# Optimization experiments

Measured on AMD Instinct MI355X. Metric: run time of the kernel, lower is better.

## Reference

```python
import jax, jax.numpy as jnp
import numpy as np

C = 128
NUM_GROUPS = 32  # min(32, 128 // 4)
EPS = 1e-6


def group_norm(x, gamma, beta):
    N, Cc, H, W = x.shape
    xg = x.reshape(N, NUM_GROUPS, -1)
    mean = xg.mean(axis=-1, keepdims=True)
    var = ((xg - mean) ** 2).mean(axis=-1, keepdims=True)
    xn = ((xg - mean) * jax.lax.rsqrt(var + EPS)).reshape(N, Cc, H, W)
    return xn * gamma[None, :, None, None] + beta[None, :, None, None]


def conv1x1(x, w, b):
    # w: [C_out, C_in], b: [C_out]; 1x1 conv == channel matmul
    return jnp.einsum('nchw,oc->nohw', x, w) + b[None, :, None, None]


def setup_inputs() -> dict:
    key = jax.random.key(0)
    ks = jax.random.split(key, 11)
    s = 1.0 / np.sqrt(C)
    return {
        'x': jax.random.normal(ks[0], (4, C, 64, 64), dtype=jnp.float32),
        'gamma': jnp.ones((C,), jnp.float32),
        'beta': jnp.zeros((C,), jnp.float32),
        'wq': jax.random.normal(ks[1], (C, C), jnp.float32) * s,
        'bq': jnp.zeros((C,), jnp.float32),
        'wk': jax.random.normal(ks[2], (C, C), jnp.float32) * s,
        'bk': jnp.zeros((C,), jnp.float32),
        'wv': jax.random.normal(ks[3], (C, C), jnp.float32) * s,
        'bv': jnp.zeros((C,), jnp.float32),
        'wo': jax.random.normal(ks[4], (C, C), jnp.float32) * s,
        'bo': jnp.zeros((C,), jnp.float32),
    }


def reference(x, gamma, beta, wq, bq, wk, bk, wv, bv, wo, bo):
    N, Cc, H, W = x.shape
    L = H * W
    xn = group_norm(x, gamma, beta)
    q = conv1x1(xn, wq, bq).reshape(N, Cc, L)  # [N,C,L]
    k = conv1x1(xn, wk, bk).reshape(N, Cc, L)
    v = conv1x1(xn, wv, bv).reshape(N, Cc, L)
    scale = 1.0 / jnp.sqrt(jnp.asarray(Cc, x.dtype))
    scores = jnp.einsum('ncl,ncm->nlm', q, k) * scale  # [N,L,L]
    weights = jax.nn.softmax(scores, axis=-1)
    attn = jnp.einsum('nlm,ncm->ncl', weights, v).reshape(N, Cc, H, W)
    return x + conv1x1(attn, wo, bo)
```

## Files before the change

kernel.cpp:

```cpp
#include <hip/hip_runtime.h>
#include <hip/hip_bf16.h>


#define N_B 4
#define C_D 128
#define L_D 4096
#define SPLIT 4
#define KVB 128
#define FSTEPS ((L_D/SPLIT)/KVB)
#define QSCALE (0.08838834764831845f * 1.4426950408889634f)
#define FIXM 16.0f

using f32x4  = __attribute__((ext_vector_type(4))) float;
using f32x16 = __attribute__((ext_vector_type(16))) float;
using bf16x8 = __attribute__((ext_vector_type(8))) short;

static __device__ __forceinline__ unsigned short f2bf(float f){
  return (unsigned short)((__builtin_bit_cast(unsigned int, f) + 0x8000u) >> 16);
}
static __device__ __forceinline__ float bf2f(unsigned short u){
  unsigned int x = ((unsigned int)u) << 16;
  return __builtin_bit_cast(float, x);
}
static __device__ __forceinline__ unsigned int pk2(float a, float b){
  unsigned int ua = __builtin_bit_cast(unsigned int, a) + 0x8000u;
  unsigned int ub = __builtin_bit_cast(unsigned int, b) + 0x8000u;
  return __builtin_amdgcn_perm(ub, ua, 0x07060302u);
}
static __device__ __forceinline__ float exp2a(float x){
  float r; asm("v_exp_f32 %0, %1" : "=v"(r) : "v"(x)); return r;
}
static __device__ __forceinline__ void gll16(const void* g, void* l){
  __builtin_amdgcn_global_load_lds(
      (const __attribute__((address_space(1))) unsigned int*)g,
      (__attribute__((address_space(3))) unsigned int*)l, 16, 0, 0);
}

__global__ __launch_bounds__(256) void gnw_k(
    const float* __restrict__ x, float* __restrict__ stats,
    const float* __restrict__ wq, const float* __restrict__ wk,
    const float* __restrict__ wv, const float* __restrict__ wo,
    unsigned short* __restrict__ wbf)
{
  int b = blockIdx.x, t = threadIdx.x;
  if (b >= 128){
    int b2 = b - 128;
    int mat = b2 >> 4;
    const float* src = (mat == 0) ? wq : (mat == 1) ? wk : (mat == 2) ? wv : wo;
    int off = (b2 & 15) * 1024 + t * 4;
    float4 v = *(const float4*)(src + off);
    *(uint2*)(wbf + mat*16384 + off) = make_uint2(pk2(v.x, v.y), pk2(v.z, v.w));
    return;
  }
  const float4* p = (const float4*)(x + (size_t)b * (4 * L_D));
  float s = 0.f, ss = 0.f;
#pragma unroll
  for (int i = 0; i < 16; ++i){
    float4 v = p[t + i*256];
    s  += v.x + v.y + v.z + v.w;
    ss += v.x*v.x + v.y*v.y + v.z*v.z + v.w*v.w;
  }
#pragma unroll
  for (int off = 32; off > 0; off >>= 1){
    s  += __shfl_down(s, off);
    ss += __shfl_down(ss, off);
  }
  __shared__ float rs4[4], rss4[4];
  if ((t & 63) == 0){ rs4[t>>6] = s; rss4[t>>6] = ss; }
  __syncthreads();
  if (t == 0){
    s  = rs4[0]+rs4[1]+rs4[2]+rs4[3];
    ss = rss4[0]+rss4[1]+rss4[2]+rss4[3];
    float mean = s * (1.f/16384.f);
    float var  = ss * (1.f/16384.f) - mean*mean;
    if (var < 0.f) var = 0.f;
    stats[2*b]   = mean;
    stats[2*b+1] = rsqrtf(var + 1e-6f);
  }
}

__global__ __launch_bounds__(256) void qkv_k(
    const float* __restrict__ x, const float* __restrict__ stats,
    const float* __restrict__ gamma, const float* __restrict__ beta,
    const unsigned short* __restrict__ wbf,
    const float* __restrict__ bq, const float* __restrict__ bk,
    const float* __restrict__ bv,
    unsigned short* __restrict__ q_ws, unsigned short* __restrict__ k_ws,
    unsigned short* __restrict__ v_ws)
{
  __shared__ unsigned short xnT[64][136];
  __shared__ unsigned short qbuf[64][136];

  int t = threadIdx.x, b = blockIdx.x;
  int wi = b >> 8;
  int bt = b & 255;
  int n = bt >> 6, l0 = (bt & 63) * 64;

  {
    int l = t & 63, cq = t >> 6;
#pragma unroll
    for (int it = 0; it < 8; ++it){
      int c0 = cq*4 + it*16;
      int g  = c0 >> 2;
      float mean = stats[(n*32+g)*2];
      float rstd = stats[(n*32+g)*2+1];
      float vv[4];
#pragma unroll
      for (int jj = 0; jj < 4; ++jj){
        int c = c0 + jj;
        float sc = rstd * gamma[c];
        float bs = beta[c] - mean * sc;
        vv[jj] = x[(size_t)(n*C_D + c)*L_D + l0 + l]*sc + bs;
      }
      *(unsigned int*)&xnT[l][c0]   = pk2(vv[0], vv[1]);
      *(unsigned int*)&xnT[l][c0+2] = pk2(vv[2], vv[3]);
    }
  }
  __syncthreads();

  int w = t >> 6, lane = t & 63, u = lane >> 4, l15 = lane & 15;
  int wc = w >> 1, wl = w & 1;
  const unsigned short* W = wbf + wi*16384;
  const float* Bv = (wi == 0) ? bq : (wi == 1) ? bk : bv;

  f32x4 zz = {0.f,0.f,0.f,0.f};
  f32x4 acc[4][2];
#pragma unroll
  for (int ct = 0; ct < 4; ++ct)
#pragma unroll
    for (int lt = 0; lt < 2; ++lt) acc[ct][lt] = zz;

#pragma unroll
  for (int kst = 0; kst < 4; ++kst){
    bf16x8 bfrag[2];
#pragma unroll
    for (int lt = 0; lt < 2; ++lt)
      bfrag[lt] = *(const bf16x8*)&xnT[32*wl + 16*lt + l15][kst*32 + 8*u];
#pragma unroll
    for (int ct = 0; ct < 4; ++ct){
      bf16x8 af = *(const bf16x8*)(W + (size_t)(64*wc + 16*ct + l15)*C_D + kst*32 + 8*u);
#pragma unroll
      for (int lt = 0; lt < 2; ++lt)
        acc[ct][lt] = __builtin_amdgcn_mfma_f32_16x16x32_bf16(af, bfrag[lt], acc[ct][lt], 0, 0, 0);
    }
  }

  if (wi < 2){
    float qs = (wi == 0) ? QSCALE : 1.0f;
#pragma unroll
    for (int ct = 0; ct < 4; ++ct){
      float bias[4];
#pragma unroll
      for (int r = 0; r < 4; ++r) bias[r] = Bv[64*wc + 16*ct + 4*u + r];
#pragma unroll
      for (int lt = 0; lt < 2; ++lt){
        float v0 = (acc[ct][lt][0] + bias[0]) * qs;
        float v1 = (acc[ct][lt][1] + bias[1]) * qs;
        float v2 = (acc[ct][lt][2] + bias[2]) * qs;
        float v3 = (acc[ct][lt][3] + bias[3]) * qs;
        int row = 32*wl + 16*lt + l15;
        int col = 64*wc + 16*ct + 4*u;
        *(unsigned int*)&qbuf[row][col]   = pk2(v0, v1);
        *(unsigned int*)&qbuf[row][col+2] = pk2(v2, v3);
      }
    }
    __syncthreads();
    {
      int l = t >> 2, ch = t & 3;
      unsigned short* dst = ((wi == 0) ? q_ws : k_ws) + (size_t)(n*L_D + l0 + l)*C_D + ch*32;
#pragma unroll
      for (int i = 0; i < 4; ++i)
        *(uint4*)(dst + i*8) = *(const uint4*)&qbuf[l][ch*32 + i*8];
    }
  } else {
    int p16 = (l15 & 3) | ((l15 & 4) << 1) | ((l15 & 8) >> 1);
#pragma unroll
    for (int ct = 0; ct < 4; ++ct){
      float bias[4];
#pragma unroll
      for (int r = 0; r < 4; ++r) bias[r] = Bv[64*wc + 16*ct + 4*u + r];
#pragma unroll
      for (int lt = 0; lt < 2; ++lt)
#pragma unroll
        for (int r = 0; r < 4; ++r){
          int co = 64*wc + 16*ct + 4*u + r;
          v_ws[(size_t)(n*C_D + co)*L_D + l0 + 32*wl + 16*lt + p16] =
              f2bf(acc[ct][lt][r] + bias[r]);
        }
    }
  }
}

__global__ __launch_bounds__(512, 2) void flash_split_k(
    const unsigned short* __restrict__ q_ws, const unsigned short* __restrict__ k_ws,
    const unsigned short* __restrict__ v_ws,
    unsigned short* __restrict__ po_ws, float* __restrict__ md_ws)
{
  __shared__ __align__(16) char shmem[131072];

  int t = threadIdx.x;
  int phys = blockIdx.x;
  int xcd = phys & 7, j = phys >> 3;
  int pair = xcd*8 + (j & 7);
  int s = j >> 3;
  int n = pair >> 4, lt256 = pair & 15;
  int l0 = lt256 * 256;
  int m_base = s * (L_D / SPLIT);
  int w = t >> 6, lane = t & 63, hi = lane >> 5, l31 = lane & 31;
  int lr = lane >> 4, ls = lane & 15;

  bf16x8 qf[8];
  {
    const unsigned short* qrow = q_ws + ((size_t)(n*L_D + l0 + 32*w + l31))*C_D;
#pragma unroll
    for (int kst = 0; kst < 8; ++kst)
      qf[kst] = *(const bf16x8*)(qrow + 16*kst + 8*hi);
  }

  f32x16 zz16;
#pragma unroll
  for (int i = 0; i < 16; ++i) zz16[i] = 0.f;
  f32x16 accO[4];
#pragma unroll
  for (int ct = 0; ct < 4; ++ct) accO[ct] = zz16;
  float rsum = 0.f;

  const unsigned short* kg[4];
  const unsigned short* vg[4];
  int ldof[4];
#pragma unroll
  for (int i = 0; i < 4; ++i){
    int row = 16*w + 4*i + lr;
    int ub = (ls << 4) ^ ((row & 15) << 4);
    kg[i] = k_ws + ((size_t)(n*L_D + m_base + row))*C_D + (ub >> 1);
    vg[i] = v_ws + ((size_t)(n*C_D + row))*L_D + m_base + (ub >> 1);
    ldof[i] = (16*w + 4*i)*256;
  }

  {
#pragma unroll
    for (int i = 0; i < 4; ++i){
      gll16(kg[i], shmem + ldof[i]);
      gll16(vg[i], shmem + 65536 + ldof[i]);
    }
  }
  __syncthreads();

#pragma unroll 2
  for (int step = 0; step < FSTEPS; ++step){
    int cur = step & 1, nxt = cur ^ 1;
    char* kB = shmem + (cur << 15);
    char* vB = shmem + 65536 + (cur << 15);

    if (step + 1 < FSTEPS){
      char* kN = shmem + (nxt << 15);
      char* vN = shmem + 65536 + (nxt << 15);
#pragma unroll
      for (int i = 0; i < 4; ++i){
        gll16(kg[i] + (size_t)(step+1)*KVB*C_D, kN + ldof[i]);
        gll16(vg[i] + (step+1)*KVB,             vN + ldof[i]);
      }
    }

    f32x16 accS[4];
#pragma unroll
    for (int mt = 0; mt < 4; ++mt) accS[mt] = zz16;
    __builtin_amdgcn_s_setprio(1);
#pragma unroll
    for (int mt = 0; mt < 4; ++mt){
      int row = 32*mt + l31;
      bf16x8 afr[8];
#pragma unroll
      for (int kst = 0; kst < 8; ++kst)
        afr[kst] = *(const bf16x8*)(kB + row*256 + ((32*kst + 16*hi) ^ ((row & 15) << 4)));
#pragma unroll
      for (int kst = 0; kst < 8; ++kst)
        accS[mt] = __builtin_amdgcn_mfma_f32_32x32x16_bf16(afr[kst], qf[kst], accS[mt], 0, 0, 0);
    }
    __builtin_amdgcn_s_setprio(0);

    union { unsigned int u[8]; bf16x8 h[2]; } Wm[4];
#pragma unroll
    for (int mt = 0; mt < 4; ++mt){
      float p[16];
#pragma unroll
      for (int r = 0; r < 16; ++r){ p[r] = exp2a(accS[mt][r] - FIXM); rsum += p[r]; }
#pragma unroll
      for (int wd = 0; wd < 8; ++wd) Wm[mt].u[wd] = pk2(p[2*wd], p[2*wd+1]);
    }

    __builtin_amdgcn_s_setprio(1);
#pragma unroll
    for (int sl = 0; sl < 8; ++sl){
      bf16x8 pf = Wm[sl >> 1].h[sl & 1];
      bf16x8 vfr[4];
#pragma unroll
      for (int ct = 0; ct < 4; ++ct){
        int vr = 32*ct + l31;
        vfr[ct] = *(const bf16x8*)(vB + vr*256 + ((32*sl + 16*hi) ^ ((vr & 15) << 4)));
      }
#pragma unroll
      for (int ct = 0; ct < 4; ++ct)
        accO[ct] = __builtin_amdgcn_mfma_f32_32x32x16_bf16(vfr[ct], pf, accO[ct], 0, 0, 0);
    }
    __builtin_amdgcn_s_setprio(0);
    __syncthreads();
  }

  rsum += __shfl_xor(rsum, 32);

  char* tB = shmem;
  {
    int lloc = 32*w + l31;
    int tsw = (lloc & 15) << 4;
    char* tr = tB + (size_t)lloc*256;
#pragma unroll
    for (int ct = 0; ct < 4; ++ct)
#pragma unroll
      for (int q = 0; q < 4; ++q){
        int cb2 = 64*ct + 16*q + 8*hi;
        *(unsigned int*)(tr + ((cb2    ) ^ tsw)) = pk2(accO[ct][4*q+0], accO[ct][4*q+1]);
        *(unsigned int*)(tr + ((cb2 + 4) ^ tsw)) = pk2(accO[ct][4*q+2], accO[ct][4*q+3]);
      }
  }
  __syncthreads();
  {
    int row2 = t >> 1, hf2 = t & 1;
    int tile = row2 >> 7, lrow = row2 & 127;
    size_t pb = ((size_t)((n*32 + 2*lt256 + tile)*SPLIT + s)) * (size_t)(128*128);
    unsigned short* dst = po_ws + pb + (size_t)lrow*128 + hf2*64;
    const char* srcr = tB + row2*256;
    int sw2 = (row2 & 15) << 4;
#pragma unroll
    for (int i = 0; i < 8; ++i)
      *(uint4*)(dst + 8*i) = *(const uint4*)(srcr + ((hf2*128 + 16*i) ^ sw2));
  }
  if (lane < 32){
    int lg = 32*w + lane;
    int tile2 = lg >> 7, lrow2 = lg & 127;
    size_t mb2 = ((size_t)((n*32 + 2*lt256 + tile2)*SPLIT + s)) * 128;
    md_ws[mb2 + lrow2] = rsum;
  }
}

__global__ __launch_bounds__(256) void combine_k(
    const unsigned short* __restrict__ po_ws, const float* __restrict__ md_ws,
    const float* __restrict__ x, const unsigned short* __restrict__ wo_bf,
    const float* __restrict__ bo, float* __restrict__ out)
{
  __shared__ __align__(16) char aB[16384];

  int t = threadIdx.x, b = blockIdx.x;
  int xcd = b & 7, j = b >> 3;
  int pair = xcd*8 + (j & 7);
  int quarter = j >> 3;
  int n = pair >> 4, lt256 = pair & 15;
  int lt64 = lt256*4 + quarter;
  int f = lt64 >> 1, loff = (lt64 & 1)*64, l0 = lt64*64;
  size_t pbase = ((size_t)((n*32 + f)*SPLIT)) * (size_t)(128*128);
  size_t mbase = ((size_t)((n*32 + f)*SPLIT)) * 128;

  {
    int l = t >> 2, q = t & 3;
    float Dg = 0.f;
#pragma unroll
    for (int s2 = 0; s2 < SPLIT; ++s2)
      Dg += md_ws[mbase + s2*128 + loff + l];
    float inv = 1.0f / Dg;

    float a[32];
#pragma unroll
    for (int i = 0; i < 32; ++i) a[i] = 0.f;
#pragma unroll
    for (int s2 = 0; s2 < SPLIT; ++s2){
      const uint4* p = (const uint4*)(po_ws + pbase + (size_t)s2*(128*128)
                                      + (size_t)(loff + l)*128 + q*32);
#pragma unroll
      for (int i = 0; i < 4; ++i){
        uint4 uv = p[i];
        unsigned int uu[4] = {uv.x, uv.y, uv.z, uv.w};
#pragma unroll
        for (int j2 = 0; j2 < 4; ++j2){
          a[8*i + 2*j2]     += bf2f((unsigned short)(uu[j2] & 0xffffu));
          a[8*i + 2*j2 + 1] += bf2f((unsigned short)(uu[j2] >> 16));
        }
      }
    }
    char* ar = aB + l*256;
    int asw = (l & 7) << 4;
#pragma unroll
    for (int i = 0; i < 16; ++i){
      int cb = q*64 + 4*i;
      *(unsigned int*)(ar + (cb ^ asw)) = pk2(a[2*i]*inv, a[2*i+1]*inv);
    }
  }
  __syncthreads();

  int w = t >> 6, lane = t & 63, hi = lane >> 5, l31 = lane & 31;
  int lh = w >> 1, ch = w & 1;
  f32x16 acc[2];
#pragma unroll
  for (int ci = 0; ci < 2; ++ci)
#pragma unroll
    for (int i = 0; i < 16; ++i) acc[ci][i] = 0.f;

#pragma unroll
  for (int kst = 0; kst < 8; ++kst){
    int row = 32*lh + l31;
    bf16x8 bfg = *(const bf16x8*)(aB + row*256 + ((32*kst + 16*hi) ^ ((row & 7) << 4)));
#pragma unroll
    for (int ci = 0; ci < 2; ++ci){
      bf16x8 af = *(const bf16x8*)(wo_bf + (size_t)(64*ch + 32*ci + l31)*C_D + 16*kst + 8*hi);
      acc[ci] = __builtin_amdgcn_mfma_f32_32x32x16_bf16(af, bfg, acc[ci], 0, 0, 0);
    }
  }
#pragma unroll
  for (int ci = 0; ci < 2; ++ci)
#pragma unroll
    for (int r = 0; r < 16; ++r){
      int o = 64*ch + 32*ci + (r & 3) + 8*(r >> 2) + 4*hi;
      size_t idx = (size_t)(n*C_D + o)*L_D + l0 + 32*lh + l31;
      out[idx] = x[idx] + bo[o] + acc[ci][r];
    }
}

extern "C" void kernel_launch(void* const* d_in, const int* in_sizes, int n_in,
                              void* d_out, int out_size, void* d_ws, size_t ws_size,
                              hipStream_t stream) {
  const float* x     = (const float*)d_in[0];
  const float* gamma = (const float*)d_in[1];
  const float* beta  = (const float*)d_in[2];
  const float* wq    = (const float*)d_in[3];
  const float* bq    = (const float*)d_in[4];
  const float* wk    = (const float*)d_in[5];
  const float* bk    = (const float*)d_in[6];
  const float* wv    = (const float*)d_in[7];
  const float* bv    = (const float*)d_in[8];
  const float* wo    = (const float*)d_in[9];
  const float* bo    = (const float*)d_in[10];
  float* out = (float*)d_out;

  char* ws = (char*)d_ws;
  float* stats          = (float*)ws;
  unsigned short* q_ws  = (unsigned short*)(ws + 4096);
  unsigned short* k_ws  = q_ws + (size_t)N_B * L_D * C_D;
  unsigned short* v_ws  = k_ws + (size_t)N_B * L_D * C_D;
  unsigned short* po_ws = v_ws + (size_t)N_B * L_D * C_D;
  float* md_ws          = (float*)(po_ws + (size_t)N_B * 32 * SPLIT * 128 * 128);
  unsigned short* wbf   = (unsigned short*)(md_ws + (size_t)N_B * 32 * SPLIT * 128);

  gnw_k<<<192, 256, 0, stream>>>(x, stats, wq, wk, wv, wo, wbf);
  qkv_k<<<768, 256, 0, stream>>>(x, stats, gamma, beta, wbf, bq, bk, bv,
                                 q_ws, k_ws, v_ws);
  flash_split_k<<<256, 512, 0, stream>>>(q_ws, k_ws, v_ws, po_ws, md_ws);
  combine_k<<<256, 256, 0, stream>>>(po_ws, md_ws, x, wbf + 3*16384, bo, out);
}
```

Before: 73.77 us.

## Halve KV tile and use four-stage ring buffer with deeper prefetch

Shrinks the K/V tile from 128 to 64 rows and replaces double buffering with a 4-slot ring that prefetches three tiles ahead. Full __syncthreads is replaced by partial vmcnt waits plus a raw barrier, so in-flight loads are not drained every step. The V tile layout in LDS is repacked so that 128 channels fit into 64-column rows. The intent is to hide global-load latency better, at the cost of twice as many loop iterations and barriers. Redundant clamped prefetches at the tail also add some memory traffic.

```diff
diff --git a/kernel.cpp b/kernel.cpp
--- a/kernel.cpp
+++ b/kernel.cpp
@@ -6,7 +6,7 @@
 #define C_D 128
 #define L_D 4096
 #define SPLIT 4
-#define KVB 128
+#define KVB 64
 #define FSTEPS ((L_D/SPLIT)/KVB)
 #define QSCALE (0.08838834764831845f * 1.4426950408889634f)
 #define FIXM 16.0f
@@ -225,49 +225,55 @@
   for (int ct = 0; ct < 4; ++ct) accO[ct] = zz16;
   float rsum = 0.f;
 
-  const unsigned short* kg[4];
-  const unsigned short* vg[4];
-  int ldof[4];
-#pragma unroll
-  for (int i = 0; i < 4; ++i){
-    int row = 16*w + 4*i + lr;
+  const unsigned short* kg[2];
+  const unsigned short* vg[2];
+  int ldof[2];
+#pragma unroll
+  for (int i = 0; i < 2; ++i){
+    int row = 8*w + 4*i + lr;
     int ub = (ls << 4) ^ ((row & 15) << 4);
     kg[i] = k_ws + ((size_t)(n*L_D + m_base + row))*C_D + (ub >> 1);
-    vg[i] = v_ws + ((size_t)(n*C_D + row))*L_D + m_base + (ub >> 1);
-    ldof[i] = (16*w + 4*i)*256;
-  }
-
-  {
-#pragma unroll
-    for (int i = 0; i < 4; ++i){
-      gll16(kg[i], shmem + ldof[i]);
-      gll16(vg[i], shmem + 65536 + ldof[i]);
-    }
-  }
-  __syncthreads();
-
-#pragma unroll 2
+    int c    = row + ((ub >> 7) << 6);
+    int mloc = (ub & 127) >> 1;
+    vg[i] = v_ws + ((size_t)(n*C_D + c))*L_D + m_base + mloc;
+    ldof[i] = (8*w + 4*i)*256;
+  }
+
+#pragma unroll
+  for (int pre = 0; pre < 3; ++pre){
+    char* kD = shmem + (pre << 14);
+    char* vD = shmem + 65536 + (pre << 14);
+    gll16(kg[0] + (size_t)pre*KVB*C_D, kD + ldof[0]);
+    gll16(kg[1] + (size_t)pre*KVB*C_D, kD + ldof[1]);
+    gll16(vg[0] + pre*KVB, vD + ldof[0]);
+    gll16(vg[1] + pre*KVB, vD + ldof[1]);
+  }
+  asm volatile("s_waitcnt vmcnt(8)" ::: "memory");
+  __builtin_amdgcn_s_barrier();
+  asm volatile("" ::: "memory");
+
+#pragma unroll 4
   for (int step = 0; step < FSTEPS; ++step){
-    int cur = step & 1, nxt = cur ^ 1;
-    char* kB = shmem + (cur << 15);
-    char* vB = shmem + 65536 + (cur << 15);
-
-    if (step + 1 < FSTEPS){
-      char* kN = shmem + (nxt << 15);
-      char* vN = shmem + 65536 + (nxt << 15);
-#pragma unroll
-      for (int i = 0; i < 4; ++i){
-        gll16(kg[i] + (size_t)(step+1)*KVB*C_D, kN + ldof[i]);
-        gll16(vg[i] + (step+1)*KVB,             vN + ldof[i]);
-      }
-    }
-
-    f32x16 accS[4];
-#pragma unroll
-    for (int mt = 0; mt < 4; ++mt) accS[mt] = zz16;
+    int pf = step + 3; if (pf >= FSTEPS) pf = FSTEPS - 1;
+    int pb = (step + 3) & 3;
+    {
+      char* kN = shmem + (pb << 14);
+      char* vN = shmem + 65536 + (pb << 14);
+      gll16(kg[0] + (size_t)pf*KVB*C_D, kN + ldof[0]);
+      gll16(kg[1] + (size_t)pf*KVB*C_D, kN + ldof[1]);
+      gll16(vg[0] + pf*KVB, vN + ldof[0]);
+      gll16(vg[1] + pf*KVB, vN + ldof[1]);
+    }
+
+    char* kB = shmem + ((step & 3) << 14);
+    char* vB = shmem + 65536 + ((step & 3) << 14);
+
+    f32x16 accS[2];
+#pragma unroll
+    for (int mt = 0; mt < 2; ++mt) accS[mt] = zz16;
     __builtin_amdgcn_s_setprio(1);
 #pragma unroll
-    for (int mt = 0; mt < 4; ++mt){
+    for (int mt = 0; mt < 2; ++mt){
       int row = 32*mt + l31;
       bf16x8 afr[8];
 #pragma unroll
@@ -279,33 +285,44 @@
     }
     __builtin_amdgcn_s_setprio(0);
 
-    union { unsigned int u[8]; bf16x8 h[2]; } Wm[4];
-#pragma unroll
-    for (int mt = 0; mt < 4; ++mt){
+    union { unsigned int u[8]; bf16x8 h[2]; } Wm[2];
+#pragma unroll
+    for (int mt = 0; mt < 2; ++mt){
       float p[16];
 #pragma unroll
-      for (int r = 0; r < 16; ++r){ p[r] = exp2a(accS[mt][r] - FIXM); rsum += p[r]; }
+      for (int r = 0; r < 16; ++r) p[r] = exp2a(accS[mt][r] - FIXM);
+      float s0 = (p[0]+p[1])+(p[2]+p[3]),   s1 = (p[4]+p[5])+(p[6]+p[7]);
+      float s2 = (p[8]+p[9])+(p[10]+p[11]), s3 = (p[12]+p[13])+(p[14]+p[15]);
+      rsum += (s0+s1)+(s2+s3);
 #pragma unroll
       for (int wd = 0; wd < 8; ++wd) Wm[mt].u[wd] = pk2(p[2*wd], p[2*wd+1]);
     }
 
     __builtin_amdgcn_s_setprio(1);
 #pragma unroll
-    for (int sl = 0; sl < 8; ++sl){
-      bf16x8 pf = Wm[sl >> 1].h[sl & 1];
+    for (int sl = 0; sl < 4; ++sl){
+      bf16x8 pf2 = Wm[sl >> 1].h[sl & 1];
       bf16x8 vfr[4];
 #pragma unroll
       for (int ct = 0; ct < 4; ++ct){
-        int vr = 32*ct + l31;
-        vfr[ct] = *(const bf16x8*)(vB + vr*256 + ((32*sl + 16*hi) ^ ((vr & 15) << 4)));
+        int c = 32*ct + l31, vrow = c & 63;
+        int lb = ((c >> 6) << 7) + 32*sl + 16*hi;
+        vfr[ct] = *(const bf16x8*)(vB + vrow*256 + (lb ^ ((vrow & 15) << 4)));
       }
 #pragma unroll
       for (int ct = 0; ct < 4; ++ct)
-        accO[ct] = __builtin_amdgcn_mfma_f32_32x32x16_bf16(vfr[ct], pf, accO[ct], 0, 0, 0);
+        accO[ct] = __builtin_amdgcn_mfma_f32_32x32x16_bf16(vfr[ct], pf2, accO[ct], 0, 0, 0);
     }
     __builtin_amdgcn_s_setprio(0);
-    __syncthreads();
-  }
+
+    asm volatile("s_waitcnt vmcnt(8)" ::: "memory");
+    __builtin_amdgcn_s_barrier();
+    asm volatile("" ::: "memory");
+  }
+
+  asm volatile("s_waitcnt vmcnt(0)" ::: "memory");
+  __builtin_amdgcn_s_barrier();
+  asm volatile("" ::: "memory");
 
   rsum += __shfl_xor(rsum, 32);
 
```

Result: no change. 73.52 us (-0.3%).
